# Kernel tuning notes

Measured on AMD Instinct MI355X. Metric: run time of the kernel, lower is better.

The kernel has to match this reference:

```python
import jax, jax.numpy as jnp
import numpy as np

B, T, N, CIN, C, L, NC, S = 8, 64, 200, 200, 128, 2, 2, 100
SPARSITY = 30


def bn(x, g, b, eps=1e-5):
    # BatchNorm1d forward with batch statistics (training-mode math, biased var)
    m = x.mean(0)
    v = x.var(0)
    return (x - m) / jnp.sqrt(v + eps) * g + b


def ln(x, g, b, eps=1e-5):
    m = x.mean(-1, keepdims=True)
    v = x.var(-1, keepdims=True)
    return (x - m) / jnp.sqrt(v + eps) * g + b


def setup_inputs() -> dict:
    key = jax.random.key(0)
    ks = iter(jax.random.split(key, 64))

    def nrm(shape, s=0.02):
        return jax.random.normal(next(ks), shape, jnp.float32) * s

    return dict(
        fMRI_v=jax.random.normal(next(ks), (B, T, N, CIN), jnp.float32),
        fMRI_a=jax.random.uniform(next(ks), (B, T, N, N), jnp.float32),
        sMRI_trad=jax.random.normal(next(ks), (B, S), jnp.float32),
        sMRI_deep=jnp.zeros((B, 1, 8, 8, 8), jnp.float32),
        csatt=1, CA_MOD=0,
        w_init=nrm((CIN, C)), b_init=jnp.zeros((C,), jnp.float32),
        gin_eps=jnp.zeros((L,), jnp.float32),
        gin_w1=nrm((L, C, C)), gin_b1=jnp.zeros((L, C), jnp.float32),
        gin_bn1_g=jnp.ones((L, C), jnp.float32), gin_bn1_b=jnp.zeros((L, C), jnp.float32),
        gin_w2=nrm((L, C, C)), gin_b2=jnp.zeros((L, C), jnp.float32),
        gin_bn2_g=jnp.ones((L, C), jnp.float32), gin_bn2_b=jnp.zeros((L, C), jnp.float32),
        sero_w=nrm((L, C, C)), sero_b=jnp.zeros((L, C), jnp.float32),
        sero_bn_g=jnp.ones((L, C), jnp.float32), sero_bn_b=jnp.zeros((L, C), jnp.float32),
        sero_aw=nrm((L, C, N)), sero_ab=jnp.zeros((L, N), jnp.float32),
        tr_wqkv=nrm((L, C, 3 * C)), tr_bqkv=jnp.zeros((L, 3 * C), jnp.float32),
        tr_wo=nrm((L, C, C)), tr_bo=jnp.zeros((L, C), jnp.float32),
        tr_ln1_g=jnp.ones((L, C), jnp.float32), tr_ln1_b=jnp.zeros((L, C), jnp.float32),
        tr_ln2_g=jnp.ones((L, C), jnp.float32), tr_ln2_b=jnp.zeros((L, C), jnp.float32),
        tr_w1=nrm((L, C, 2 * C)), tr_b1=jnp.zeros((L, 2 * C), jnp.float32),
        tr_w2=nrm((L, 2 * C, C)), tr_b2=jnp.zeros((L, C), jnp.float32),
        cls_w=nrm((L, C, NC)), cls_b=jnp.zeros((L, NC), jnp.float32),
        smri_w=nrm((S, C)), smri_b=jnp.zeros((C,), jnp.float32),
        smri_bn_g=jnp.ones((C,), jnp.float32), smri_bn_b=jnp.zeros((C,), jnp.float32),
    )


def reference(fMRI_v, fMRI_a, sMRI_trad, sMRI_deep, csatt, CA_MOD,
              w_init, b_init, gin_eps,
              gin_w1, gin_b1, gin_bn1_g, gin_bn1_b,
              gin_w2, gin_b2, gin_bn2_g, gin_bn2_b,
              sero_w, sero_b, sero_bn_g, sero_bn_b, sero_aw, sero_ab,
              tr_wqkv, tr_bqkv, tr_wo, tr_bo,
              tr_ln1_g, tr_ln1_b, tr_ln2_g, tr_ln2_b,
              tr_w1, tr_b1, tr_w2, tr_b2,
              cls_w, cls_b, smri_w, smri_b, smri_bn_g, smri_bn_b):
    b, t, n = fMRI_a.shape[:3]
    # initial linear over flattened (b t n) tokens
    h3 = (fMRI_v.reshape(-1, fMRI_v.shape[-1]) @ w_init + b_init).reshape(b, t, n, -1)
    # _collate_adjacency: per-(sample,timepoint) percentile threshold -> block-diag sparse
    # with all-ones values; equivalent to a batched masked matmul.
    thr = jnp.percentile(fMRI_a, 100 - SPARSITY, axis=(-2, -1), keepdims=True)
    mask = (fMRI_a > thr).astype(h3.dtype)  # [b,t,n,n]

    logit = jnp.zeros((b, cls_w.shape[-1]), h3.dtype)
    latents, node_attns, time_attns = [], [], []
    scale = 1.0 / jnp.sqrt(jnp.asarray(h3.shape[-1], h3.dtype))
    for l in range(L):
        # LayerGIN: note the original feeds h3 (initial features) to EVERY layer
        agg = jnp.einsum('btij,btjc->btic', mask, h3) + gin_eps[l] * h3
        x = agg.reshape(-1, agg.shape[-1])
        x = jax.nn.relu(bn(x @ gin_w1[l] + gin_b1[l], gin_bn1_g[l], gin_bn1_b[l]))
        x = jax.nn.relu(bn(x @ gin_w2[l] + gin_b2[l], gin_bn2_g[l], gin_bn2_b[l]))
        hb = x.reshape(b, t, n, -1).transpose(1, 0, 2, 3)  # (t,b,n,c)
        # ModuleSERO readout (node_axis=2)
        xr = hb.mean(2)  # (t,b,c)
        e = jax.nn.gelu(bn(xr.reshape(t * b, -1) @ sero_w[l] + sero_b[l],
                           sero_bn_g[l], sero_bn_b[l]), approximate=False)
        ga = jax.nn.sigmoid(e @ sero_aw[l] + sero_ab[l]).reshape(t, b, n)
        hr = (hb * ga[..., None]).mean(2)  # (t,b,c)
        node_attns.append(ga.transpose(1, 0, 2))  # (b,t,n)
        # ModuleTransformer (single head, post-LN, no residual before ln1)
        qkv = hr @ tr_wqkv[l] + tr_bqkv[l]
        q, k, v = jnp.split(qkv, 3, axis=-1)
        A = jax.nn.softmax(jnp.einsum('tbc,sbc->bts', q, k) * scale, axis=-1)  # (b,t,t)
        att = jnp.einsum('bts,sbc->tbc', A, v) @ tr_wo[l] + tr_bo[l]
        x1 = ln(att, tr_ln1_g[l], tr_ln1_b[l])
        m = jax.nn.relu(x1 @ tr_w1[l] + tr_b1[l]) @ tr_w2[l] + tr_b2[l]
        x2 = ln(x1 + m, tr_ln2_g[l], tr_ln2_b[l])
        time_attns.append(A)
        lat = x2.sum(0)  # cls_token='sum' over time
        logit = logit + lat @ cls_w[l] + cls_b[l]
        latents.append(lat)
    feat_fMRI = jnp.stack(latents, 1).mean(1)  # (b,c)
    feat_sMRI = bn(sMRI_trad @ smri_w + smri_b, smri_bn_g, smri_bn_b)
    node_attn = jnp.stack(node_attns, 1)  # (b,L,t,n)
    time_attn = jnp.stack(time_attns, 1)  # (b,L,t,t)
    return (logit, feat_fMRI, feat_sMRI, node_attn, time_attn)
```

## Files before the change

### kernel.cpp

```cpp
#include <hip/hip_runtime.h>
#include <math.h>

#define B_   8
#define T_   64
#define N_   200
#define CIN_ 200
#define C_   128
#define L_   2
#define NC_  2
#define S_   100
#define BT_  512
#define RB_  102400

#define ACT_NONE 0
#define ACT_RELU 1
#define ACT_GELU 2

typedef __attribute__((ext_vector_type(8))) short short8v;
typedef __attribute__((ext_vector_type(4))) float f32x4v;

union U4S8 { uint4 u; short8v s; };

__device__ __forceinline__ unsigned short f2bf(float f) {
    unsigned u = __float_as_uint(f);
// ... 75 lines not shown
                    float f = vv[j];
                    if (p < 6144) { candV[p] = f; candP[p] = (unsigned short)(i4 * 4 + j); }
                    int bin = (int)((f - 0.65f) * 10240.0f);
                    bin = bin < 0 ? 0 : (bin > 1023 ? 1023 : bin);
                    atomicAdd(&hist[bin], 1);
                    p++;
                }
            }
        }
    }
    red[tid] = c_lo;
    __syncthreads();
    for (int off = 512; off; off >>= 1) {
        if (tid < off) red[tid] += red[tid + off];
        __syncthreads();
    }
    int c_lo_tot = red[0];
    if (tid < 256) part[tid] = hist[4*tid] + hist[4*tid+1] + hist[4*tid+2] + hist[4*tid+3];
    __syncthreads();
    if (tid < 32) {
        int s = 0;
        for (int i = 0; i < 8; i++) s += part[8*tid + i];
        grp[tid] = s;
    }
    __syncthreads();
    if (tid == 0) {
        int r = 27999 - c_lo_tot;
        int cum = 0, g = 0;
        while (cum + grp[g] <= r) cum += grp[g++];
        int t = g * 8;
        while (cum + part[t] <= r) cum += part[t++];
        int b = t * 4;
        while (cum + hist[b] <= r) cum += hist[b++];
        meta[2] = b; meta[3] = cum;
        int r1 = r + 1;
        cum = 0; g = 0;
        while (cum + grp[g] <= r1) cum += grp[g++];
        t = g * 8;
        while (cum + part[t] <= r1) cum += part[t++];
        b = t * 4;
        while (cum + hist[b] <= r1) cum += hist[b++];
        meta[4] = b; meta[5] = r;
    }
    __syncthreads();
    int blo = meta[2], base = meta[3], bhi = meta[4], r = meta[5];
    int m = meta[0]; if (m > 6144) m = 6144;
    for (int i = tid; i < m; i += 1024) {
        float v = candV[i];
        int bin = (int)((v - 0.65f) * 10240.0f);
        bin = bin < 0 ? 0 : (bin > 1023 ? 1023 : bin);
        if (bin >= blo && bin <= bhi) {
            int p = atomicAdd(&meta[1], 1);
            if (p < 256) cand2[p] = v;
        }
    }
    __syncthreads();
    if (tid == 0) {
        int m2 = meta[1]; if (m2 > 256) m2 = 256;
        for (int i = 1; i < m2; i++) {
            float key = cand2[i]; int j = i - 1;
            while (j >= 0 && cand2[j] > key) { cand2[j+1] = cand2[j]; j--; }
            cand2[j+1] = key;
        }
        float s1 = cand2[r - base], s2 = cand2[r + 1 - base];
        float tv = s1 * 0.701171875f + s2 * 0.298828125f;
        thr[bt] = tv;
        s_thr = tv;
    }
    __syncthreads();
    float tv = s_thr;
    for (int i = tid; i < m; i += 1024) {
        if (candV[i] > tv) {
            int vi = candP[i];
            int row = vi / 200, col = vi - row * 200;
            atomicOr(&smask[row * 7 + (col >> 5)], 1u << (col & 31));
        }
    }
    __syncthreads();
    for (int i = tid; i < 1400; i += 1024)
        msk[(long)bt * 1400 + i] = smask[i];
}

__global__ void wtcvt_kernel(const float* __restrict__ w, int K, int Kpad,
                             unsigned short* __restrict__ wt) {
    int c = blockIdx.x;
    for (int k = threadIdx.x; k < Kpad; k += 64) {
        float v = (k < K) ? w[(long)k * 128 + c] : 0.f;
        wt[(long)c * Kpad + k] = f2bf(v);
    }
}

template<bool A_BF16, bool BN_IN, bool BIAS_OUT, bool STATS_OUT>
__global__ __launch_bounds__(256) void gemm_direct_kernel(
        const void* __restrict__ xv, int K, int Kstride, int Ksteps,
        const unsigned short* __restrict__ wt, int Kpad,
        const float* __restrict__ bias, const float* __restrict__ statsIn,
        const float* __restrict__ bng, const float* __restrict__ bnb,
        unsigned short* __restrict__ y, float* __restrict__ statsOut) {
    constexpr int ASZ  = A_BF16 ? 8192 : 16384;
    constexpr int BOFF = 2 * ASZ;
    constexpr int NEED = 2 * ASZ + 2 * 8192;
    constexpr int POOL = NEED > 32768 ? NEED : 32768;
    __shared__ unsigned char pool[POOL];
    __shared__ float bnS[128], bnB[128];
    int tid = threadIdx.x;
    if (BN_IN) {
        if (tid < 128) {
            float mm = statsIn[tid] * (1.f / (float)RB_);
            float var = fmaxf(statsIn[128 + tid] * (1.f / (float)RB_) - mm * mm, 0.f);
            float sc = bng[tid] / sqrtf(var + 1e-5f);
            bnS[tid] = sc; bnB[tid] = bnb[tid] - mm * sc;
        }
    }
    int wave = tid >> 6, lane = tid & 63, quad = lane >> 4, m16 = lane & 15;
    long row0g = (long)blockIdx.x * 128;

    auto STAGE = [&](int buf, int ks) {
        #pragma unroll
        for (int j = 0; j < 2; j++) {
            int r = j * 64 + (tid >> 2);
            int c = (tid & 3) ^ ((r >> 1) & 3);
            const char* src = (const char*)wt + (long)r * (Kpad * 2) + ks * 64 + c * 16;
            char* dst = (char*)pool + BOFF + buf * 8192 + j * 4096 + wave * 1024;
            GLL(src, dst);
        }
        if (A_BF16) {
            const char* xb = (const char*)xv;
            #pragma unroll
            for (int j = 0; j < 2; j++) {
                int r = j * 64 + (tid >> 2);
                int c = (tid & 3) ^ ((r >> 1) & 3);
                const char* src = xb + ((row0g + r) * Kstride + ks * 32) * 2 + c * 16;
                char* dst = (char*)pool + buf * ASZ + j * 4096 + wave * 1024;
                GLL(src, dst);
            }
        } else {
            const char* xb = (const char*)xv;
            #pragma unroll
            for (int j = 0; j < 4; j++) {
                int r = j * 32 + (tid >> 3);
                int c = (tid & 7) ^ (r & 7);
                const char* src = xb + ((row0g + r) * Kstride + ks * 32) * 4 + c * 16;
                char* dst = (char*)pool + buf * ASZ + j * 4096 + wave * 1024;
                GLL(src, dst);
            }
        }
    };

    f32x4v acc[2][8];
    #pragma unroll
    for (int i = 0; i < 2; i++)
        #pragma unroll
        for (int j = 0; j < 8; j++) acc[i][j] = (f32x4v){0.f, 0.f, 0.f, 0.f};

    STAGE(0, 0);
    __syncthreads();

    for (int ks = 0; ks < Ksteps; ks++) {
        if (ks + 1 < Ksteps) {
            STAGE((ks + 1) & 1, ks + 1);
            if (A_BF16) asm volatile("s_waitcnt vmcnt(4)" ::: "memory");
            else        asm volatile("s_waitcnt vmcnt(6)" ::: "memory");
        } else {
            asm volatile("s_waitcnt vmcnt(0)" ::: "memory");
        }
        __builtin_amdgcn_s_barrier();
        asm volatile("" ::: "memory");

        const char* Ab = (const char*)pool + (ks & 1) * ASZ;
        const char* Bb = (const char*)pool + BOFF + (ks & 1) * 8192;
        int kf = ks * 32 + quad * 8;
        U4S8 bU[8];
        #pragma unroll
        for (int nt = 0; nt < 8; nt++) {
            int r = nt * 16 + m16;
            int ch = quad ^ ((r >> 1) & 3);
            bU[nt].u = *(const uint4*)(Bb + r * 64 + ch * 16);
        }
        U4S8 aU[2];
        if (A_BF16) {
            #pragma unroll
            for (int mt = 0; mt < 2; mt++) {
                int r = wave * 32 + mt * 16 + m16;
                int ch = quad ^ ((r >> 1) & 3);
                aU[mt].u = *(const uint4*)(Ab + r * 64 + ch * 16);
            }
            if (BN_IN) {
                float4 s0 = *(const float4*)&bnS[kf], s1 = *(const float4*)&bnS[kf + 4];
                float4 b0 = *(const float4*)&bnB[kf], b1 = *(const float4*)&bnB[kf + 4];
                #pragma unroll
                for (int mt = 0; mt < 2; mt++) {
                    uint4 u = aU[mt].u;
                    float f0 = fmaxf(bflo(u.x) * s0.x + b0.x, 0.f);
                    float f1 = fmaxf(bfhi(u.x) * s0.y + b0.y, 0.f);
                    float f2 = fmaxf(bflo(u.y) * s0.z + b0.z, 0.f);
                    float f3 = fmaxf(bfhi(u.y) * s0.w + b0.w, 0.f);
                    float f4 = fmaxf(bflo(u.z) * s1.x + b1.x, 0.f);
                    float f5 = fmaxf(bfhi(u.z) * s1.y + b1.y, 0.f);
                    float f6 = fmaxf(bflo(u.w) * s1.z + b1.z, 0.f);
                    float f7 = fmaxf(bfhi(u.w) * s1.w + b1.w, 0.f);
                    u.x = packbf(f0, f1); u.y = packbf(f2, f3);
                    u.z = packbf(f4, f5); u.w = packbf(f6, f7);
                    aU[mt].u = u;
                }
            }
        } else {
            #pragma unroll
            for (int mt = 0; mt < 2; mt++) {
                int r = wave * 32 + mt * 16 + m16;
                int swz = r & 7;
                const char* base = Ab + r * 128;
                float4 v0 = *(const float4*)(base + ((2 * quad) ^ swz) * 16);
                float4 v1 = *(const float4*)(base + ((2 * quad + 1) ^ swz) * 16);
                uint4 o;
                o.x = packbf(v0.x, v0.y); o.y = packbf(v0.z, v0.w);
                o.z = packbf(v1.x, v1.y); o.w = packbf(v1.z, v1.w);
                aU[mt].u = o;
            }
        }
        #pragma unroll
        for (int nt = 0; nt < 8; nt++) {
            acc[0][nt] = __builtin_amdgcn_mfma_f32_16x16x32_bf16(aU[0].s, bU[nt].s, acc[0][nt], 0, 0, 0);
            acc[1][nt] = __builtin_amdgcn_mfma_f32_16x16x32_bf16(aU[1].s, bU[nt].s, acc[1][nt], 0, 0, 0);
        }
        asm volatile("s_waitcnt lgkmcnt(0)" ::: "memory");
        __builtin_amdgcn_s_barrier();
        asm volatile("" ::: "memory");
    }
    if (!A_BF16 && (K & 31) != 0) {
        int kf = Ksteps * 32 + quad * 8;
        U4S8 bU[8];
        #pragma unroll
        for (int nt = 0; nt < 8; nt++)
            bU[nt].u = *(const uint4*)&wt[(long)(nt * 16 + m16) * Kpad + kf];
        U4S8 aU[2];
        const float* x = (const float*)xv;
        #pragma unroll
        for (int mt = 0; mt < 2; mt++) {
            uint4 o = {0u, 0u, 0u, 0u};
            if (kf + 8 <= K) {
                const float* p = &x[(row0g + wave * 32 + mt * 16 + m16) * Kstride + kf];
                float4 v0 = *(const float4*)p;
                float4 v1 = *(const float4*)(p + 4);
                o.x = packbf(v0.x, v0.y); o.y = packbf(v0.z, v0.w);
                o.z = packbf(v1.x, v1.y); o.w = packbf(v1.z, v1.w);
            }
            aU[mt].u = o;
        }
        #pragma unroll
        for (int nt = 0; nt < 8; nt++) {
            acc[0][nt] = __builtin_amdgcn_mfma_f32_16x16x32_bf16(aU[0].s, bU[nt].s, acc[0][nt], 0, 0, 0);
            acc[1][nt] = __builtin_amdgcn_mfma_f32_16x16x32_bf16(aU[1].s, bU[nt].s, acc[1][nt], 0, 0, 0);
        }
    }

    unsigned short* trans = (unsigned short*)pool;
    float sAcc[8], qAcc[8];
    #pragma unroll
    for (int nt = 0; nt < 8; nt++) {
        int col = nt * 16 + m16;
        float bv = BIAS_OUT ? bias[col] : 0.f;
        float s = 0.f, q = 0.f;
        #pragma unroll
        for (int mt = 0; mt < 2; mt++) {
            int lrb = wave * 32 + mt * 16 + quad * 4;
            #pragma unroll
            for (int i = 0; i < 4; i++) {
                int lr = lrb + i;
                float v = acc[mt][nt][i] + bv;
                trans[lr * 128 + (col ^ ((lr & 6) << 2))] = f2bf(v);
                if (STATS_OUT) { s += v; q += v * v; }
            }
        }
        sAcc[nt] = s; qAcc[nt] = q;
    }
    __syncthreads();
    #pragma unroll
    for (int rnd = 0; rnd < 8; rnd++) {
        int row = rnd * 16 + (tid >> 4), ch = tid & 15;
        uint4 v = *(const uint4*)&trans[row * 128 + ((ch * 8) ^ ((row & 6) << 2))];
        *(uint4*)&y[(row0g + row) * 128 + ch * 8] = v;
    }
    if (STATS_OUT) {
        __syncthreads();
        float* redS = (float*)pool;
        float* redQ = redS + 2048;
        #pragma unroll
        for (int nt = 0; nt < 8; nt++) {
            int col = nt * 16 + m16;
            redS[col * 16 + wave * 4 + quad] = sAcc[nt];
            redQ[col * 16 + wave * 4 + quad] = qAcc[nt];
        }
        __syncthreads();
        if (tid < 128) {
            float s = 0.f, q = 0.f;
            #pragma unroll
            for (int j = 0; j < 16; j++) { s += redS[tid * 16 + j]; q += redQ[tid * 16 + j]; }
            atomicAdd(&statsOut[tid], s);
            atomicAdd(&statsOut[128 + tid], q);
        }
    }
}

__global__ __launch_bounds__(256) void gemmT_kernel(
        const unsigned short* __restrict__ xb, const unsigned short* __restrict__ wt,
        unsigned short* __restrict__ zt) {
    __shared__ unsigned char pool[32768];
    int tid = threadIdx.x;
    int wave = tid >> 6, lane = tid & 63, quad = lane >> 4, m16 = lane & 15;
    long row0g = (long)blockIdx.x * 128;

    auto STAGE = [&](int buf, int ks) {
        #pragma unroll
        for (int j = 0; j < 2; j++) {
            int r = j * 64 + (tid >> 2);
            int c = (tid & 3) ^ ((r >> 1) & 3);
            const char* srcB = (const char*)wt + (long)r * 256 + ks * 64 + c * 16;
            char* dstB = (char*)pool + 16384 + buf * 8192 + j * 4096 + wave * 1024;
            GLL(srcB, dstB);
            const char* srcA = (const char*)xb + ((row0g + r) * 128 + ks * 32) * 2 + c * 16;
            char* dstA = (char*)pool + buf * 8192 + j * 4096 + wave * 1024;
            GLL(srcA, dstA);
        }
    };

    f32x4v acc[2][8];
    #pragma unroll
    for (int i = 0; i < 2; i++)
        #pragma unroll
        for (int j = 0; j < 8; j++) acc[i][j] = (f32x4v){0.f, 0.f, 0.f, 0.f};

    STAGE(0, 0);
    __syncthreads();

    for (int ks = 0; ks < 4; ks++) {
        if (ks < 3) {
            STAGE((ks + 1) & 1, ks + 1);
            asm volatile("s_waitcnt vmcnt(4)" ::: "memory");
        } else {
            asm volatile("s_waitcnt vmcnt(0)" ::: "memory");
        }
        __builtin_amdgcn_s_barrier();
        asm volatile("" ::: "memory");

        const char* Ab = (const char*)pool + (ks & 1) * 8192;
        const char* Bb = (const char*)pool + 16384 + (ks & 1) * 8192;
        U4S8 bU[8];
        #pragma unroll
        for (int nt = 0; nt < 8; nt++) {
            int r = nt * 16 + m16;
            int ch = quad ^ ((r >> 1) & 3);
            bU[nt].u = *(const uint4*)(Bb + r * 64 + ch * 16);
        }
        U4S8 aU[2];
        #pragma unroll
        for (int mt = 0; mt < 2; mt++) {
            int r = wave * 32 + mt * 16 + m16;
            int ch = quad ^ ((r >> 1) & 3);
            aU[mt].u = *(const uint4*)(Ab + r * 64 + ch * 16);
        }
        #pragma unroll
        for (int nt = 0; nt < 8; nt++) {
            acc[0][nt] = __builtin_amdgcn_mfma_f32_16x16x32_bf16(aU[0].s, bU[nt].s, acc[0][nt], 0, 0, 0);
            acc[1][nt] = __builtin_amdgcn_mfma_f32_16x16x32_bf16(aU[1].s, bU[nt].s, acc[1][nt], 0, 0, 0);
        }
        asm volatile("s_waitcnt lgkmcnt(0)" ::: "memory");
        __builtin_amdgcn_s_barrier();
        asm volatile("" ::: "memory");
    }
    unsigned short* tile = (unsigned short*)pool;
    #pragma unroll
    for (int nt = 0; nt < 8; nt++) {
        int col = nt * 16 + m16;
        #pragma unroll
        for (int mt = 0; mt < 2; mt++) {
            int lrb = wave * 32 + mt * 16 + quad * 4;
            #pragma unroll
            for (int i = 0; i < 4; i++) {
                int lr = lrb + i;
                tile[lr * 128 + (col ^ ((lr & 14) << 2))] = f2bf(acc[mt][nt][i]);
            }
        }
    }
    __syncthreads();
    int r0 = blockIdx.x * 128;
    int bt0 = r0 / 200, n0 = r0 - bt0 * 200;
    int len0 = 200 - n0; if (len0 > 128) len0 = 128;
    int c = tid & 127, h = tid >> 7;
    #pragma unroll
    for (int u = 0; u < 8; u++) {
        int rl = h * 64 + u * 8;
        unsigned short e[8];
        #pragma unroll
        for (int j = 0; j < 8; j++)
            e[j] = tile[(rl + j) * 128 + (c ^ (((rl + j) & 14) << 2))];
        uint4 o;
        o.x = (unsigned)e[0] | ((unsigned)e[1] << 16);
        o.y = (unsigned)e[2] | ((unsigned)e[3] << 16);
        o.z = (unsigned)e[4] | ((unsigned)e[5] << 16);
        o.w = (unsigned)e[6] | ((unsigned)e[7] << 16);
        int bt, n;
        if (rl < len0) { bt = bt0; n = n0 + rl; } else { bt = bt0 + 1; n = rl - len0; }
        *(uint4*)&zt[((long)bt * 128 + c) * 224 + n] = o;
    }
    if (n0 >= 72) {
        uint4 z = {0u, 0u, 0u, 0u};
        for (int idx = tid; idx < 384; idx += 256) {
            int c2 = idx & 127, u2 = idx >> 7;
            *(uint4*)&zt[((long)bt0 * 128 + c2) * 224 + 200 + u2 * 8] = z;
        }
    }
}

__global__ __launch_bounds__(256) void maskagg_kernel(
        const unsigned* __restrict__ msk, const unsigned short* __restrict__ zt,
        const float* __restrict__ geps, int l, const float* __restrict__ b1,
        unsigned short* __restrict__ y, float* __restrict__ statsOut) {
    __shared__ union {
        unsigned short stage[4][4096];
        unsigned short trans[16384];
        struct { float S[2048]; float Q[2048]; } red;
    } u;
    __shared__ unsigned sbits[128 * 7];
    int tid = threadIdx.x;
    int bt = blockIdx.x & 511, half = blockIdx.x >> 9;
    int row0 = half * 128;
    int wave = tid >> 6, lane = tid & 63, quad = lane >> 4, m16 = lane & 15;
    const char* ztb = (const char*)(zt + (long)bt * 128 * 224);

    int sr = tid >> 2, sq = tid & 3;
    auto STAGE = [&](int buf, int kc) {
        #pragma unroll
        for (int j = 0; j < 2; j++) {
            int r = j * 64 + sr;
            int q = sq ^ ((r >> 1) & 3);
            const char* src = ztb + r * 448 + kc * 64 + q * 16;
            char* dst = (char*)&u.stage[buf][0] + j * 4096 + wave * 1024;
            GLL(src, dst);
        }
    };

    STAGE(0, 0); STAGE(1, 1); STAGE(2, 2);
    for (int idx = tid; idx < 896; idx += 256) {
        int gr = row0 + idx / 7;
        sbits[idx] = (gr < N_) ? msk[(long)bt * 1400 + gr * 7 + (idx % 7)] : 0u;
    }
    float eps = geps[l];
    unsigned ONEu = 0x3F80u;
    unsigned E0 = (unsigned)f2bf(eps), E1 = (unsigned)f2bf(1.f + eps);

    f32x4v acc[2][8];
    #pragma unroll
    for (int i = 0; i < 2; i++)
        #pragma unroll
        for (int j = 0; j < 8; j++) acc[i][j] = (f32x4v){0.f, 0.f, 0.f, 0.f};

    __syncthreads();

    for (int kc = 0; kc < 7; kc++) {
        if (kc < 4) STAGE((kc + 3) & 3, kc + 3);
        if (kc == 3)      asm volatile("s_waitcnt vmcnt(6)" ::: "memory");
        else if (kc == 4) asm volatile("s_waitcnt vmcnt(4)" ::: "memory");
        else if (kc == 5) asm volatile("s_waitcnt vmcnt(2)" ::: "memory");
        else if (kc == 6) asm volatile("s_waitcnt vmcnt(0)" ::: "memory");
        __builtin_amdgcn_s_barrier();
        asm volatile("" ::: "memory");

        const char* sb = (const char*)&u.stage[kc & 3][0];
        int kf = kc * 32 + quad * 8;
        U4S8 bU[8];
        #pragma unroll
        for (int nt = 0; nt < 8; nt++) {
            int r = nt * 16 + m16;
            int q = quad ^ ((r >> 1) & 3);
            bU[nt].u = *(const uint4*)(sb + r * 64 + q * 16);
        }
        U4S8 aU[2];
        #pragma unroll
        for (int mt = 0; mt < 2; mt++) {
            int lr = wave * 32 + mt * 16 + m16;
            unsigned bits = (sbits[lr * 7 + kc] >> (quad * 8)) & 0xFFu;
            int gr = row0 + lr;
            unsigned o[4];
            #pragma unroll
            for (int p = 0; p < 4; p++) {
                int j0 = 2 * p, j1 = 2 * p + 1;
                unsigned lo = ((bits >> j0) & 1u) ? ONEu : 0u;
                unsigned hi = ((bits >> j1) & 1u) ? ONEu : 0u;
                if (gr == kf + j0) lo = ((bits >> j0) & 1u) ? E1 : E0;
                if (gr == kf + j1) hi = ((bits >> j1) & 1u) ? E1 : E0;
                o[p] = lo | (hi << 16);
            }
            aU[mt].u = make_uint4(o[0], o[1], o[2], o[3]);
        }
        #pragma unroll
        for (int nt = 0; nt < 8; nt++) {
            acc[0][nt] = __builtin_amdgcn_mfma_f32_16x16x32_bf16(aU[0].s, bU[nt].s, acc[0][nt], 0, 0, 0);
            acc[1][nt] = __builtin_amdgcn_mfma_f32_16x16x32_bf16(aU[1].s, bU[nt].s, acc[1][nt], 0, 0, 0);
        }
        asm volatile("s_waitcnt lgkmcnt(0)" ::: "memory");
        __builtin_amdgcn_s_barrier();
        asm volatile("" ::: "memory");
    }

    float sAcc[8], qAcc[8];
    #pragma unroll
    for (int nt = 0; nt < 8; nt++) {
        int col = nt * 16 + m16;
        float bv = b1[col];
        float s = 0.f, q = 0.f;
        #pragma unroll
        for (int mt = 0; mt < 2; mt++) {
            int lrb = wave * 32 + mt * 16 + quad * 4;
            #pragma unroll
            for (int i = 0; i < 4; i++) {
                int lr = lrb + i;
                float v = acc[mt][nt][i] + bv;
                u.trans[lr * 128 + (col ^ ((lr & 6) << 2))] = f2bf(v);
                if (row0 + lr < N_) { s += v; q += v * v; }
            }
        }
        sAcc[nt] = s; qAcc[nt] = q;
    }
    __syncthreads();
    #pragma unroll
    for (int rnd = 0; rnd < 8; rnd++) {
        int row = rnd * 16 + (tid >> 4), ch = tid & 15;
        int gr = row0 + row;
        uint4 v = *(const uint4*)&u.trans[row * 128 + ((ch * 8) ^ ((row & 6) << 2))];
        if (gr < N_)
            *(uint4*)&y[((long)bt * N_ + gr) * 128 + ch * 8] = v;
    }
    __syncthreads();
    #pragma unroll
    for (int nt = 0; nt < 8; nt++) {
        int col = nt * 16 + m16;
        u.red.S[col * 16 + wave * 4 + quad] = sAcc[nt];
        u.red.Q[col * 16 + wave * 4 + quad] = qAcc[nt];
    }
    __syncthreads();
    if (tid < 128) {
        float s = 0.f, q = 0.f;
        #pragma unroll
        for (int j = 0; j < 16; j++) { s += u.red.S[tid * 16 + j]; q += u.red.Q[tid * 16 + j]; }
        atomicAdd(&statsOut[tid], s);
        atomicAdd(&statsOut[128 + tid], q);
    }
}

__global__ __launch_bounds__(128) void xr2_kernel(const unsigned short* __restrict__ raw,
                                                  const float* __restrict__ stats,
                                                  const float* __restrict__ g,
                                                  const float* __restrict__ b,
                                                  float* __restrict__ xr) {
    int t = blockIdx.x / B_, bb = blockIdx.x % B_;
    const unsigned short* base = raw + ((long)bb * T_ + t) * N_ * C_;
    int c = threadIdx.x;
    float m = stats[c] * (1.f / (float)RB_);
    float var = fmaxf(stats[128 + c] * (1.f / (float)RB_) - m * m, 0.f);
    float sc = g[c] / sqrtf(var + 1e-5f);
    float sh = b[c] - m * sc;
    float s = 0.f;
    for (int n = 0; n < N_; n++) s += fmaxf(fmaf(bf2f(base[n * C_ + c]), sc, sh), 0.f);
    xr[(long)blockIdx.x * C_ + c] = s * (1.f / 200.f);
}

__global__ __launch_bounds__(128) void hr2_kernel(const unsigned short* __restrict__ raw,
                                                  const float* __restrict__ stats,
                                                  const float* __restrict__ g,
                                                  const float* __restrict__ b,
                                                  const float* __restrict__ ga,
                                                  float* __restrict__ hr) {
    __shared__ float sga[N_];
    int t = blockIdx.x / B_, bb = blockIdx.x % B_;
    const unsigned short* base = raw + ((long)bb * T_ + t) * N_ * C_;
    for (int i = threadIdx.x; i < N_; i += blockDim.x) sga[i] = ga[(long)blockIdx.x * N_ + i];
    __syncthreads();
    int c = threadIdx.x;
    float m = stats[c] * (1.f / (float)RB_);
    float var = fmaxf(stats[128 + c] * (1.f / (float)RB_) - m * m, 0.f);
    float sc = g[c] / sqrtf(var + 1e-5f);
    float sh = b[c] - m * sc;
    float s = 0.f;
    for (int n = 0; n < N_; n++)
        s = fmaf(fmaxf(fmaf(bf2f(base[n * C_ + c]), sc, sh), 0.f), sga[n], s);
    hr[(long)blockIdx.x * C_ + c] = s * (1.f / 200.f);
}

template<int K, int ROWS, bool STATS>
__global__ void mm_kernel(const float* __restrict__ x, const float* __restrict__ w,
                          const float* __restrict__ bias, float* __restrict__ y,
                          int Cout, int act, float* __restrict__ stats) {
    __shared__ float sx[ROWS * K];
    long r0 = (long)blockIdx.x * ROWS;
    for (int idx = threadIdx.x; idx < ROWS * K; idx += blockDim.x)
        sx[idx] = x[r0 * K + idx];
    __syncthreads();
    int c = threadIdx.x;
    float acc[ROWS];
    #pragma unroll
    for (int i = 0; i < ROWS; i++) acc[i] = 0.f;
    for (int k = 0; k < K; k++) {
        float wv = w[k * Cout + c];
        #pragma unroll
        for (int i = 0; i < ROWS; i++) acc[i] = fmaf(sx[i * K + k], wv, acc[i]);
    }
    float bv = bias ? bias[c] : 0.f;
    float s = 0.f, ss = 0.f;
    for (int i = 0; i < ROWS; i++) {
        float vv = acc[i] + bv;
        if (act == ACT_RELU) vv = fmaxf(vv, 0.f);
        y[(r0 + i) * Cout + c] = vv;
        if (STATS) { s += vv; ss += vv * vv; }
    }
    if (STATS) {
        atomicAdd(&stats[c], s);
        atomicAdd(&stats[C_ + c], ss);
    }
}

__global__ __launch_bounds__(256) void ga_kernel(const float* __restrict__ eRaw,
                          const float* __restrict__ stats,
                          const float* __restrict__ sg, const float* __restrict__ sb,
                          const float* __restrict__ aw, const float* __restrict__ ab,
                          float* __restrict__ ga, float* __restrict__ node_out, int l) {
    __shared__ float sx[4 * C_];
    __shared__ float bnS[C_], bnB[C_];
    int tid = threadIdx.x;
    if (tid < C_) {
        float m = stats[tid] * (1.f / (float)BT_);
        float var = fmaxf(stats[C_ + tid] * (1.f / (float)BT_) - m * m, 0.f);
        float inv = 1.f / sqrtf(var + 1e-5f);
        float sc = inv * sg[tid];
        bnS[tid] = sc;
        bnB[tid] = sb[tid] - m * sc;
    }
    __syncthreads();
    long r0 = (long)blockIdx.x * 4;
    for (int idx = tid; idx < 4 * C_; idx += 256) {
        int col = idx & (C_ - 1);
        float v = eRaw[r0 * C_ + idx] * bnS[col] + bnB[col];
        sx[idx] = 0.5f * v * (1.f + erff(v * 0.70710678118654752f));
    }
    __syncthreads();
    int c = tid;
    if (c < N_) {
        float acc[4] = {0.f, 0.f, 0.f, 0.f};
        for (int k = 0; k < C_; k++) {
            float wv = aw[k * N_ + c];
            #pragma unroll
            for (int i = 0; i < 4; i++) acc[i] = fmaf(sx[i * C_ + k], wv, acc[i]);
        }
        float bv = ab[c];
        for (int i = 0; i < 4; i++) {
            int tb = (int)r0 + i;
            int t = tb / B_, b = tb % B_;
            float v = 1.f / (1.f + expf(-(acc[i] + bv)));
            ga[(long)tb * N_ + c] = v;
            node_out[(((long)b * L_ + l) * T_ + t) * N_ + c] = v;
        }
    }
}

__global__ __launch_bounds__(128) void attnav_kernel(const float* __restrict__ qkv,
                            float* __restrict__ time_out, float* __restrict__ attv, int l) {
    __shared__ float q[C_];
    __shared__ float sa[T_];
    int tid = threadIdx.x;
    int t = blockIdx.x / B_, b = blockIdx.x % B_;
    q[tid] = qkv[((long)t * B_ + b) * 384 + tid];
    __syncthreads();
    if (tid < 64) {
        const float* krow = qkv + ((long)tid * B_ + b) * 384 + C_;
        float s = 0.f;
        for (int c = 0; c < C_; c++) s = fmaf(q[c], krow[c], s);
        s *= 0.08838834764831843f;
        float mx = s;
        #pragma unroll
        for (int off = 32; off; off >>= 1) mx = fmaxf(mx, __shfl_xor(mx, off));
        float e = expf(s - mx), sum = e;
        #pragma unroll
        for (int off = 32; off; off >>= 1) sum += __shfl_xor(sum, off);
        float p = e / sum;
        sa[tid] = p;
        time_out[(((long)b * L_ + l) * T_ + t) * T_ + tid] = p;
    }
    __syncthreads();
    float s2 = 0.f;
    for (int sp = 0; sp < T_; sp++)
        s2 = fmaf(sa[sp], qkv[((long)sp * B_ + b) * 384 + 256 + tid], s2);
    attv[((long)t * B_ + b) * C_ + tid] = s2;
}

__global__ __launch_bounds__(128) void mmln_kernel(const float* __restrict__ x,
                          const float* __restrict__ w, const float* __restrict__ bias,
                          const float* __restrict__ g, const float* __restrict__ bb,
                          float* __restrict__ out) {
    __shared__ float sx[2 * C_];
    __shared__ float red[C_];
    int tid = threadIdx.x;
    long r0 = (long)blockIdx.x * 2;
    sx[tid]       = x[r0 * C_ + tid];
    sx[C_ + tid]  = x[r0 * C_ + C_ + tid];
    __syncthreads();
    float a0 = 0.f, a1 = 0.f;
    for (int k = 0; k < C_; k++) {
        float wv = w[k * C_ + tid];
        a0 = fmaf(sx[k], wv, a0);
        a1 = fmaf(sx[C_ + k], wv, a1);
    }
    float bv = bias[tid];
    float v[2] = {a0 + bv, a1 + bv};
    #pragma unroll 1
    for (int r = 0; r < 2; r++) {
        red[tid] = v[r]; __syncthreads();
        for (int off = 64; off; off >>= 1) { if (tid < off) red[tid] += red[tid + off]; __syncthreads(); }
        float m = red[0] * (1.f / C_); __syncthreads();
        float d = v[r] - m;
        red[tid] = d * d; __syncthreads();
        for (int off = 64; off; off >>= 1) { if (tid < off) red[tid] += red[tid + off]; __syncthreads(); }
        float var = red[0] * (1.f / C_); __syncthreads();
        out[(r0 + r) * C_ + tid] = d * (1.f / sqrtf(var + 1e-5f)) * g[tid] + bb[tid];
    }
}

__global__ __launch_bounds__(256) void ffn_kernel(const float* __restrict__ x1,
                          const float* __restrict__ w1, const float* __restrict__ b1,
                          const float* __restrict__ w2, const float* __restrict__ b2,
                          const float* __restrict__ g, const float* __restrict__ bb,
                          float* __restrict__ out) {
    __shared__ float sx[2 * C_];
    __shared__ float mid[2 * 256];
    __shared__ float red[C_];
    int tid = threadIdx.x;
    long r0 = (long)blockIdx.x * 2;
    sx[tid] = x1[r0 * C_ + tid];
    __syncthreads();
    float a0 = 0.f, a1 = 0.f;
    for (int k = 0; k < C_; k++) {
        float wv = w1[k * 256 + tid];
        a0 = fmaf(sx[k], wv, a0);
        a1 = fmaf(sx[C_ + k], wv, a1);
    }
    float bv = b1[tid];
    mid[tid]       = fmaxf(a0 + bv, 0.f);
    mid[256 + tid] = fmaxf(a1 + bv, 0.f);
    __syncthreads();
    float v[2] = {0.f, 0.f};
    if (tid < C_) {
        float c0 = 0.f, c1 = 0.f;
        for (int k = 0; k < 256; k++) {
            float wv = w2[k * C_ + tid];
            c0 = fmaf(mid[k], wv, c0);
            c1 = fmaf(mid[256 + k], wv, c1);
        }
        float bv2 = b2[tid];
        v[0] = c0 + bv2 + sx[tid];
        v[1] = c1 + bv2 + sx[C_ + tid];
    }
    #pragma unroll 1
    for (int r = 0; r < 2; r++) {
        if (tid < C_) red[tid] = v[r];
        __syncthreads();
        for (int off = 64; off; off >>= 1) { if (tid < off) red[tid] += red[tid + off]; __syncthreads(); }
        float m = red[0] * (1.f / C_); __syncthreads();
        float d = v[r] - m;
        if (tid < C_) red[tid] = d * d;
        __syncthreads();
        for (int off = 64; off; off >>= 1) { if (tid < off) red[tid] += red[tid + off]; __syncthreads(); }
        float var = red[0] * (1.f / C_); __syncthreads();
        if (tid < C_)
            out[(r0 + r) * C_ + tid] = d * (1.f / sqrtf(var + 1e-5f)) * g[tid] + bb[tid];
    }
}

__global__ void latsum_kernel(const float* __restrict__ x2, float* __restrict__ lat) {
    int b = blockIdx.x, c = threadIdx.x;
    float s = 0.f;
    for (int t = 0; t < T_; t++) s += x2[((long)t * B_ + b) * C_ + c];
    lat[(long)b * C_ + c] = s;
}

__global__ void final_kernel(const float* __restrict__ lat, const float* __restrict__ cls_w,
                             const float* __restrict__ cls_b, float* __restrict__ out) {
    int idx = blockIdx.x * blockDim.x + threadIdx.x;
    if (idx < B_ * NC_) {
        int b = idx / NC_, nc = idx % NC_;
        float s = 0.f;
        for (int l = 0; l < L_; l++) {
            float acc = 0.f;
            for (int c = 0; c < C_; c++)
                acc = fmaf(lat[l * B_ * C_ + b * C_ + c], cls_w[l * C_ * NC_ + c * NC_ + nc], acc);
            s += acc + cls_b[l * NC_ + nc];
        }
        out[idx] = s;
    } else if (idx < B_ * NC_ + B_ * C_) {
        int j = idx - B_ * NC_;
        out[idx] = 0.5f * (lat[j] + lat[B_ * C_ + j]);
    }
}

__global__ void smri_kernel(const float* __restrict__ trad, const float* __restrict__ w,
                            const float* __restrict__ bias, const float* __restrict__ g,
                            const float* __restrict__ bb, float* __restrict__ out) {
    int c = threadIdx.x;
    float y[B_];
    for (int b = 0; b < B_; b++) {
        float s = bias[c];
        for (int k = 0; k < S_; k++) s = fmaf(trad[b * S_ + k], w[k * C_ + c], s);
        y[b] = s;
    }
    float m = 0.f;
    for (int b = 0; b < B_; b++) m += y[b];
    m *= (1.f / B_);
    float var = 0.f;
    for (int b = 0; b < B_; b++) { float d = y[b] - m; var += d * d; }
    var *= (1.f / B_);
    float inv = 1.f / sqrtf(var + 1e-5f);
    for (int b = 0; b < B_; b++) out[b * C_ + c] = (y[b] - m) * inv * g[c] + bb[c];
}

extern "C" void kernel_launch(void* const* d_in, const int* in_sizes, int n_in,
                              void* d_out, int out_size, void* d_ws, size_t ws_size,
                              hipStream_t stream) {
    const float* fv       = (const float*)d_in[0];
    const float* fa       = (const float*)d_in[1];
    const float* trad     = (const float*)d_in[2];
    const float* w_init   = (const float*)d_in[6];
    const float* b_init   = (const float*)d_in[7];
    const float* gin_eps  = (const float*)d_in[8];
    const float* gin_w1   = (const float*)d_in[9];
    const float* gin_b1   = (const float*)d_in[10];
    const float* gbn1g    = (const float*)d_in[11];
    const float* gbn1b    = (const float*)d_in[12];
    const float* gin_w2   = (const float*)d_in[13];
    const float* gin_b2   = (const float*)d_in[14];
    const float* gbn2g    = (const float*)d_in[15];
    const float* gbn2b    = (const float*)d_in[16];
    const float* sero_w   = (const float*)d_in[17];
    const float* sero_b   = (const float*)d_in[18];
    const float* sbng     = (const float*)d_in[19];
    const float* sbnb     = (const float*)d_in[20];
    const float* sero_aw  = (const float*)d_in[21];
    const float* sero_ab  = (const float*)d_in[22];
    const float* wqkv     = (const float*)d_in[23];
    const float* bqkv     = (const float*)d_in[24];
    const float* wo       = (const float*)d_in[25];
    const float* bo       = (const float*)d_in[26];
    const float* ln1g     = (const float*)d_in[27];
    const float* ln1b     = (const float*)d_in[28];
    const float* ln2g     = (const float*)d_in[29];
    const float* ln2b     = (const float*)d_in[30];
    const float* tw1      = (const float*)d_in[31];
    const float* tb1      = (const float*)d_in[32];
    const float* tw2      = (const float*)d_in[33];
    const float* tb2      = (const float*)d_in[34];
    const float* cls_w    = (const float*)d_in[35];
    const float* cls_b    = (const float*)d_in[36];
    const float* smri_w   = (const float*)d_in[37];
    const float* smri_b   = (const float*)d_in[38];
    const float* smri_g   = (const float*)d_in[39];
    const float* smri_bb  = (const float*)d_in[40];

    float* out = (float*)d_out;

    const long SZ_BIG = (long)RB_ * C_;
    unsigned short* H3b = (unsigned short*)d_ws;
    unsigned short* Y1b = H3b + SZ_BIG;
    unsigned short* Y2b = Y1b + SZ_BIG;
    unsigned short* ZTb = Y2b + SZ_BIG;
    float* fbase = (float*)(ZTb + (long)BT_ * 128 * 224);
    float* THR  = fbase;
    float* STAT = THR + 512;
    float* XR   = STAT + 256;
    float* E    = XR  + BT_ * C_;
    float* GA   = E   + BT_ * C_;
    float* HR   = GA  + BT_ * N_;
    float* QKV  = HR  + BT_ * C_;
    float* ATTV = QKV + BT_ * 3 * C_;
    float* ATT  = ATTV + BT_ * C_;
    float* X1   = ATT + BT_ * C_;
    float* MMB  = X1  + BT_ * C_;
    float* X2   = MMB + BT_ * 2 * C_;
    float* LAT  = X2  + BT_ * C_;
    float* STATB = MMB;
    unsigned short* WT0 = (unsigned short*)(LAT + L_ * B_ * C_);
    unsigned short* WT1 = WT0 + 128 * 224;
    unsigned short* WT2 = WT1 + 2 * 128 * 128;
    unsigned* MSK = (unsigned*)(WT2 + 2 * 128 * 128);

    float* OUT_LOGIT = out;
    float* OUT_FEATS = out + 1040;
    float* OUT_NODE  = out + 2064;
    float* OUT_TIME  = out + 206864;

    wtcvt_kernel<<<128, 64, 0, stream>>>(w_init, 200, 224, WT0);
    wtcvt_kernel<<<128, 64, 0, stream>>>(gin_w1,           128, 128, WT1);
    wtcvt_kernel<<<128, 64, 0, stream>>>(gin_w1 + C_ * C_, 128, 128, WT1 + 128 * 128);
    wtcvt_kernel<<<128, 64, 0, stream>>>(gin_w2,           128, 128, WT2);
    wtcvt_kernel<<<128, 64, 0, stream>>>(gin_w2 + C_ * C_, 128, 128, WT2 + 128 * 128);

    gemm_direct_kernel<false, false, true, false><<<RB_ / 128, 256, 0, stream>>>(
        fv, 200, 200, 6, WT0, 224, b_init, nullptr, nullptr, nullptr, H3b, nullptr);
    thr_kernel<<<BT_, 1024, 0, stream>>>(fa, THR, MSK);

    for (int l = 0; l < L_; l++) {
        gemmT_kernel<<<RB_ / 128, 256, 0, stream>>>(H3b, WT1 + l * 128 * 128, ZTb);
        hipMemsetAsync(STAT, 0, 256 * sizeof(float), stream);
        maskagg_kernel<<<BT_ * 2, 256, 0, stream>>>(MSK, ZTb, gin_eps, l, gin_b1 + l * C_, Y2b, STAT);
        hipMemsetAsync(STATB, 0, 256 * sizeof(float), stream);
        gemm_direct_kernel<true, true, true, true><<<RB_ / 128, 256, 0, stream>>>(
            Y2b, 128, 128, 4, WT2 + l * 128 * 128, 128, gin_b2 + l * C_, STAT,
            gbn1g + l * C_, gbn1b + l * C_, Y1b, STATB);
        xr2_kernel<<<BT_, 128, 0, stream>>>(Y1b, STATB, gbn2g + l * C_, gbn2b + l * C_, XR);

        hipMemsetAsync(STAT, 0, 256 * sizeof(float), stream);
        mm_kernel<128, 2, true><<<BT_ / 2, 128, 0, stream>>>(
            XR, sero_w + l * C_ * C_, sero_b + l * C_, E, C_, ACT_NONE, STAT);
        ga_kernel<<<BT_ / 4, 256, 0, stream>>>(E, STAT, sbng + l * C_, sbnb + l * C_,
            sero_aw + l * C_ * N_, sero_ab + l * N_, GA, OUT_NODE, l);
        hr2_kernel<<<BT_, 128, 0, stream>>>(Y1b, STATB, gbn2g + l * C_, gbn2b + l * C_, GA, HR);

        mm_kernel<128, 2, false><<<BT_ / 2, 384, 0, stream>>>(
            HR, wqkv + l * C_ * 3 * C_, bqkv + l * 3 * C_, QKV, 3 * C_, ACT_NONE, nullptr);
        attnav_kernel<<<BT_, 128, 0, stream>>>(QKV, OUT_TIME, ATTV, l);
        mmln_kernel<<<BT_ / 2, 128, 0, stream>>>(ATTV, wo + l * C_ * C_, bo + l * C_,
            ln1g + l * C_, ln1b + l * C_, X1);
        ffn_kernel<<<BT_ / 2, 256, 0, stream>>>(X1, tw1 + l * C_ * 2 * C_, tb1 + l * 2 * C_,
            tw2 + l * 2 * C_ * C_, tb2 + l * C_, ln2g + l * C_, ln2b + l * C_, X2);
        latsum_kernel<<<B_, 128, 0, stream>>>(X2, LAT + l * B_ * C_);
    }

    final_kernel<<<5, 256, 0, stream>>>(LAT, cls_w, cls_b, OUT_LOGIT);
    smri_kernel<<<1, 128, 0, stream>>>(trad, smri_w, smri_b, smri_g, smri_bb, OUT_FEATS);
}
```

Before: 778.2 us.

## Aggregate node features before the GIN weight matmul and fuse it into the mask kernel

The GIN step now aggregates first, computing (A + eps·I)·H3 with the binary mask, and only then multiplies by W1, instead of computing H3·W1 first. The initial feature GEMM converts fp32 input to bf16 in-kernel and writes both the row-major and the transposed H3, which removes the per-layer transpose-GEMM launch. The W1 GEMM, the eps·H3 self term and the bias are fused into the mask-aggregation kernel, reading W1 and H3 from global memory. Separately, the two node-mean reduction kernels now use 256 threads, with each half summing 100 nodes. The tradeoff is an extra bf16 rounding of the aggregate before W1, plus uncached global loads inside the fused kernel.

```diff
diff --git a/kernel.cpp b/kernel.cpp
--- a/kernel.cpp
+++ b/kernel.cpp
@@ -401,10 +401,11 @@
     }
 }
 
-__global__ __launch_bounds__(256) void gemmT_kernel(
-        const unsigned short* __restrict__ xb, const unsigned short* __restrict__ wt,
-        unsigned short* __restrict__ zt) {
-    __shared__ unsigned char pool[32768];
+__global__ __launch_bounds__(256) void h3gemmT_kernel(
+        const float* __restrict__ xv, const unsigned short* __restrict__ wt,
+        const float* __restrict__ bias,
+        unsigned short* __restrict__ yrow, unsigned short* __restrict__ zt) {
+    __shared__ unsigned char pool[49152];
     int tid = threadIdx.x;
     int wave = tid >> 6, lane = tid & 63, quad = lane >> 4, m16 = lane & 15;
     long row0g = (long)blockIdx.x * 128;
@@ -414,12 +415,18 @@
         for (int j = 0; j < 2; j++) {
             int r = j * 64 + (tid >> 2);
             int c = (tid & 3) ^ ((r >> 1) & 3);
-            const char* srcB = (const char*)wt + (long)r * 256 + ks * 64 + c * 16;
-            char* dstB = (char*)pool + 16384 + buf * 8192 + j * 4096 + wave * 1024;
-            GLL(srcB, dstB);
-            const char* srcA = (const char*)xb + ((row0g + r) * 128 + ks * 32) * 2 + c * 16;
-            char* dstA = (char*)pool + buf * 8192 + j * 4096 + wave * 1024;
-            GLL(srcA, dstA);
+            const char* src = (const char*)wt + (long)r * 448 + ks * 64 + c * 16;
+            char* dst = (char*)pool + 32768 + buf * 8192 + j * 4096 + wave * 1024;
+            GLL(src, dst);
+        }
+        const char* xb = (const char*)xv;
+        #pragma unroll
+        for (int j = 0; j < 4; j++) {
+            int r = j * 32 + (tid >> 3);
+            int c = (tid & 7) ^ (r & 7);
+            const char* src = xb + ((row0g + r) * 200 + ks * 32) * 4 + c * 16;
+            char* dst = (char*)pool + buf * 16384 + j * 4096 + wave * 1024;
+            GLL(src, dst);
         }
     };
 
@@ -432,18 +439,18 @@
     STAGE(0, 0);
     __syncthreads();
 
-    for (int ks = 0; ks < 4; ks++) {
-        if (ks < 3) {
+    for (int ks = 0; ks < 6; ks++) {
+        if (ks + 1 < 6) {
             STAGE((ks + 1) & 1, ks + 1);
-            asm volatile("s_waitcnt vmcnt(4)" ::: "memory");
+            asm volatile("s_waitcnt vmcnt(6)" ::: "memory");
         } else {
             asm volatile("s_waitcnt vmcnt(0)" ::: "memory");
         }
         __builtin_amdgcn_s_barrier();
         asm volatile("" ::: "memory");
 
-        const char* Ab = (const char*)pool + (ks & 1) * 8192;
-        const char* Bb = (const char*)pool + 16384 + (ks & 1) * 8192;
+        const char* Ab = (const char*)pool + (ks & 1) * 16384;
+        const char* Bb = (const char*)pool + 32768 + (ks & 1) * 8192;
         U4S8 bU[8];
         #pragma unroll
         for (int nt = 0; nt < 8; nt++) {
@@ -455,8 +462,14 @@
         #pragma unroll
         for (int mt = 0; mt < 2; mt++) {
             int r = wave * 32 + mt * 16 + m16;
-            int ch = quad ^ ((r >> 1) & 3);
-            aU[mt].u = *(const uint4*)(Ab + r * 64 + ch * 16);
+            int swz = r & 7;
+            const char* base = Ab + r * 128;
+            float4 v0 = *(const float4*)(base + ((2 * quad) ^ swz) * 16);
+            float4 v1 = *(const float4*)(base + ((2 * quad + 1) ^ swz) * 16);
+            uint4 o;
+            o.x = packbf(v0.x, v0.y); o.y = packbf(v0.z, v0.w);
+            o.z = packbf(v1.x, v1.y); o.w = packbf(v1.z, v1.w);
+            aU[mt].u = o;
         }
         #pragma unroll
         for (int nt = 0; nt < 8; nt++) {
@@ -467,21 +480,54 @@
         __builtin_amdgcn_s_barrier();
         asm volatile("" ::: "memory");
     }
+    {
+        int kf = 192 + quad * 8;
+        U4S8 bU[8];
+        #pragma unroll
+        for (int nt = 0; nt < 8; nt++)
+            bU[nt].u = *(const uint4*)&wt[(long)(nt * 16 + m16) * 224 + kf];
+        U4S8 aU[2];
+        #pragma unroll
+        for (int mt = 0; mt < 2; mt++) {
+            uint4 o = {0u, 0u, 0u, 0u};
+            if (kf + 8 <= 200) {
+                const float* p = &xv[(row0g + wave * 32 + mt * 16 + m16) * 200 + kf];
+                float4 v0 = *(const float4*)p;
+                float4 v1 = *(const float4*)(p + 4);
+                o.x = packbf(v0.x, v0.y); o.y = packbf(v0.z, v0.w);
+                o.z = packbf(v1.x, v1.y); o.w = packbf(v1.z, v1.w);
+            }
+            aU[mt].u = o;
+        }
+        #pragma unroll
+        for (int nt = 0; nt < 8; nt++) {
+            acc[0][nt] = __builtin_amdgcn_mfma_f32_16x16x32_bf16(aU[0].s, bU[nt].s, acc[0][nt], 0, 0, 0);
+            acc[1][nt] = __builtin_amdgcn_mfma_f32_16x16x32_bf16(aU[1].s, bU[nt].s, acc[1][nt], 0, 0, 0);
+        }
+    }
+
     unsigned short* tile = (unsigned short*)pool;
     #pragma unroll
     for (int nt = 0; nt < 8; nt++) {
         int col = nt * 16 + m16;
+        float bv = bias[col];
         #pragma unroll
         for (int mt = 0; mt < 2; mt++) {
             int lrb = wave * 32 + mt * 16 + quad * 4;
             #pragma unroll
             for (int i = 0; i < 4; i++) {
                 int lr = lrb + i;
-                tile[lr * 128 + (col ^ ((lr & 14) << 2))] = f2bf(acc[mt][nt][i]);
-            }
-        }
-    }
-    __syncthreads();
+                tile[lr * 128 + (col ^ ((lr & 14) << 2))] = f2bf(acc[mt][nt][i] + bv);
+            }
+        }
+    }
+    __syncthreads();
+    #pragma unroll
+    for (int rnd = 0; rnd < 8; rnd++) {
+        int row = rnd * 16 + (tid >> 4), ch = tid & 15;
+        uint4 v = *(const uint4*)&tile[row * 128 + ((ch * 8) ^ ((row & 14) << 2))];
+        *(uint4*)&yrow[(row0g + row) * 128 + ch * 8] = v;
+    }
     int r0 = blockIdx.x * 128;
     int bt0 = r0 / 200, n0 = r0 - bt0 * 200;
     int len0 = 200 - n0; if (len0 > 128) len0 = 128;
@@ -511,8 +557,9 @@
     }
 }
 
-__global__ __launch_bounds__(256) void maskagg_kernel(
+__global__ __launch_bounds__(256) void maskfused_kernel(
         const unsigned* __restrict__ msk, const unsigned short* __restrict__ zt,
+        const unsigned short* __restrict__ h3, const unsigned short* __restrict__ w1t,
         const float* __restrict__ geps, int l, const float* __restrict__ b1,
         unsigned short* __restrict__ y, float* __restrict__ statsOut) {
     __shared__ union {
@@ -544,9 +591,7 @@
         int gr = row0 + idx / 7;
         sbits[idx] = (gr < N_) ? msk[(long)bt * 1400 + gr * 7 + (idx % 7)] : 0u;
     }
-    float eps = geps[l];
     unsigned ONEu = 0x3F80u;
-    unsigned E0 = (unsigned)f2bf(eps), E1 = (unsigned)f2bf(1.f + eps);
 
     f32x4v acc[2][8];
     #pragma unroll
@@ -566,7 +611,6 @@
         asm volatile("" ::: "memory");
 
         const char* sb = (const char*)&u.stage[kc & 3][0];
-        int kf = kc * 32 + quad * 8;
         U4S8 bU[8];
         #pragma unroll
         for (int nt = 0; nt < 8; nt++) {
@@ -579,15 +623,11 @@
         for (int mt = 0; mt < 2; mt++) {
             int lr = wave * 32 + mt * 16 + m16;
             unsigned bits = (sbits[lr * 7 + kc] >> (quad * 8)) & 0xFFu;
-            int gr = row0 + lr;
             unsigned o[4];
             #pragma unroll
             for (int p = 0; p < 4; p++) {
-                int j0 = 2 * p, j1 = 2 * p + 1;
-                unsigned lo = ((bits >> j0) & 1u) ? ONEu : 0u;
-                unsigned hi = ((bits >> j1) & 1u) ? ONEu : 0u;
-                if (gr == kf + j0) lo = ((bits >> j0) & 1u) ? E1 : E0;
-                if (gr == kf + j1) hi = ((bits >> j1) & 1u) ? E1 : E0;
+                unsigned lo = ((bits >> (2 * p)) & 1u) ? ONEu : 0u;
+                unsigned hi = ((bits >> (2 * p + 1)) & 1u) ? ONEu : 0u;
                 o[p] = lo | (hi << 16);
             }
             aU[mt].u = make_uint4(o[0], o[1], o[2], o[3]);
@@ -601,6 +641,63 @@
         __builtin_amdgcn_s_barrier();
         asm volatile("" ::: "memory");
     }
+
+    #pragma unroll
+    for (int nt = 0; nt < 8; nt++) {
+        int col = nt * 16 + m16;
+        #pragma unroll
+        for (int mt = 0; mt < 2; mt++) {
+            int lrb = wave * 32 + mt * 16 + quad * 4;
+            #pragma unroll
+            for (int i = 0; i < 4; i++) {
+                int lr = lrb + i;
+                u.trans[lr * 128 + (col ^ ((lr & 6) << 2))] = f2bf(acc[mt][nt][i]);
+            }
+        }
+    }
+    __syncthreads();
+
+    float eps = geps[l];
+    f32x4v acc2[2][8];
+    #pragma unroll
+    for (int i = 0; i < 2; i++)
+        #pragma unroll
+        for (int j = 0; j < 8; j++) acc2[i][j] = (f32x4v){0.f, 0.f, 0.f, 0.f};
+
+    for (int ks = 0; ks < 4; ks++) {
+        int kf = ks * 32 + quad * 8;
+        U4S8 bU[8];
+        #pragma unroll
+        for (int nt = 0; nt < 8; nt++)
+            bU[nt].u = *(const uint4*)&w1t[(long)(nt * 16 + m16) * 128 + kf];
+        U4S8 aU[2];
+        #pragma unroll
+        for (int mt = 0; mt < 2; mt++) {
+            int r = wave * 32 + mt * 16 + m16;
+            uint4 mu = *(const uint4*)&u.trans[r * 128 + (kf ^ ((r & 6) << 2))];
+            int gr = row0 + r;
+            uint4 hu = {0u, 0u, 0u, 0u};
+            if (gr < N_) hu = *(const uint4*)&h3[((long)bt * N_ + gr) * 128 + kf];
+            float f0 = bflo(mu.x) + eps * bflo(hu.x);
+            float f1 = bfhi(mu.x) + eps * bfhi(hu.x);
+            float f2 = bflo(mu.y) + eps * bflo(hu.y);
+            float f3 = bfhi(mu.y) + eps * bfhi(hu.y);
+            float f4 = bflo(mu.z) + eps * bflo(hu.z);
+            float f5 = bfhi(mu.z) + eps * bfhi(hu.z);
+            float f6 = bflo(mu.w) + eps * bflo(hu.w);
+            float f7 = bfhi(mu.w) + eps * bfhi(hu.w);
+            uint4 o;
+            o.x = packbf(f0, f1); o.y = packbf(f2, f3);
+            o.z = packbf(f4, f5); o.w = packbf(f6, f7);
+            aU[mt].u = o;
+        }
+        #pragma unroll
+        for (int nt = 0; nt < 8; nt++) {
+            acc2[0][nt] = __builtin_amdgcn_mfma_f32_16x16x32_bf16(aU[0].s, bU[nt].s, acc2[0][nt], 0, 0, 0);
+            acc2[1][nt] = __builtin_amdgcn_mfma_f32_16x16x32_bf16(aU[1].s, bU[nt].s, acc2[1][nt], 0, 0, 0);
+        }
+    }
+    __syncthreads();
 
     float sAcc[8], qAcc[8];
     #pragma unroll
@@ -614,7 +711,7 @@
             #pragma unroll
             for (int i = 0; i < 4; i++) {
                 int lr = lrb + i;
-                float v = acc[mt][nt][i] + bv;
+                float v = acc2[mt][nt][i] + bv;
                 u.trans[lr * 128 + (col ^ ((lr & 6) << 2))] = f2bf(v);
                 if (row0 + lr < N_) { s += v; q += v * v; }
             }
@@ -647,43 +744,52 @@
     }
 }
 
-__global__ __launch_bounds__(128) void xr2_kernel(const unsigned short* __restrict__ raw,
+__global__ __launch_bounds__(256) void xr2_kernel(const unsigned short* __restrict__ raw,
                                                   const float* __restrict__ stats,
                                                   const float* __restrict__ g,
                                                   const float* __restrict__ b,
                                                   float* __restrict__ xr) {
+    __shared__ float red[256];
+    int tid = threadIdx.x, c = tid & 127, hf = tid >> 7;
     int t = blockIdx.x / B_, bb = blockIdx.x % B_;
     const unsigned short* base = raw + ((long)bb * T_ + t) * N_ * C_;
-    int c = threadIdx.x;
     float m = stats[c] * (1.f / (float)RB_);
     float var = fmaxf(stats[128 + c] * (1.f / (float)RB_) - m * m, 0.f);
     float sc = g[c] / sqrtf(var + 1e-5f);
     float sh = b[c] - m * sc;
     float s = 0.f;
-    for (int n = 0; n < N_; n++) s += fmaxf(fmaf(bf2f(base[n * C_ + c]), sc, sh), 0.f);
-    xr[(long)blockIdx.x * C_ + c] = s * (1.f / 200.f);
-}
-
-__global__ __launch_bounds__(128) void hr2_kernel(const unsigned short* __restrict__ raw,
+    for (int n = hf * 100; n < hf * 100 + 100; n++)
+        s += fmaxf(fmaf(bf2f(base[n * C_ + c]), sc, sh), 0.f);
+    red[tid] = s;
+    __syncthreads();
+    if (hf == 0)
+        xr[(long)blockIdx.x * C_ + c] = (red[c] + red[c + 128]) * (1.f / 200.f);
+}
+
+__global__ __launch_bounds__(256) void hr2_kernel(const unsigned short* __restrict__ raw,
                                                   const float* __restrict__ stats,
                                                   const float* __restrict__ g,
                                                   const float* __restrict__ b,
                                                   const float* __restrict__ ga,
                                                   float* __restrict__ hr) {
     __shared__ float sga[N_];
+    __shared__ float red[256];
+    int tid = threadIdx.x, c = tid & 127, hf = tid >> 7;
     int t = blockIdx.x / B_, bb = blockIdx.x % B_;
     const unsigned short* base = raw + ((long)bb * T_ + t) * N_ * C_;
-    for (int i = threadIdx.x; i < N_; i += blockDim.x) sga[i] = ga[(long)blockIdx.x * N_ + i];
-    __syncthreads();
-    int c = threadIdx.x;
+    for (int i = tid; i < N_; i += 256) sga[i] = ga[(long)blockIdx.x * N_ + i];
+    __syncthreads();
     float m = stats[c] * (1.f / (float)RB_);
     float var = fmaxf(stats[128 + c] * (1.f / (float)RB_) - m * m, 0.f);
     float sc = g[c] / sqrtf(var + 1e-5f);
     float sh = b[c] - m * sc;
     float s = 0.f;
-    for (int n = 0; n < N_; n++)
+    for (int n = hf * 100; n < hf * 100 + 100; n++)
         s = fmaf(fmaxf(fmaf(bf2f(base[n * C_ + c]), sc, sh), 0.f), sga[n], s);
-    hr[(long)blockIdx.x * C_ + c] = s * (1.f / 200.f);
+    red[tid] = s;
+    __syncthreads();
+    if (hf == 0)
+        hr[(long)blockIdx.x * C_ + c] = (red[c] + red[c + 128]) * (1.f / 200.f);
 }
 
 template<int K, int ROWS, bool STATS>
@@ -999,26 +1105,25 @@
     wtcvt_kernel<<<128, 64, 0, stream>>>(gin_w2,           128, 128, WT2);
     wtcvt_kernel<<<128, 64, 0, stream>>>(gin_w2 + C_ * C_, 128, 128, WT2 + 128 * 128);
 
-    gemm_direct_kernel<false, false, true, false><<<RB_ / 128, 256, 0, stream>>>(
-        fv, 200, 200, 6, WT0, 224, b_init, nullptr, nullptr, nullptr, H3b, nullptr);
+    h3gemmT_kernel<<<RB_ / 128, 256, 0, stream>>>(fv, WT0, b_init, H3b, ZTb);
     thr_kernel<<<BT_, 1024, 0, stream>>>(fa, THR, MSK);
 
     for (int l = 0; l < L_; l++) {
-        gemmT_kernel<<<RB_ / 128, 256, 0, stream>>>(H3b, WT1 + l * 128 * 128, ZTb);
         hipMemsetAsync(STAT, 0, 256 * sizeof(float), stream);
-        maskagg_kernel<<<BT_ * 2, 256, 0, stream>>>(MSK, ZTb, gin_eps, l, gin_b1 + l * C_, Y2b, STAT);
+        maskfused_kernel<<<BT_ * 2, 256, 0, stream>>>(MSK, ZTb, H3b, WT1 + l * 128 * 128,
+            gin_eps, l, gin_b1 + l * C_, Y2b, STAT);
         hipMemsetAsync(STATB, 0, 256 * sizeof(float), stream);
         gemm_direct_kernel<true, true, true, true><<<RB_ / 128, 256, 0, stream>>>(
             Y2b, 128, 128, 4, WT2 + l * 128 * 128, 128, gin_b2 + l * C_, STAT,
             gbn1g + l * C_, gbn1b + l * C_, Y1b, STATB);
-        xr2_kernel<<<BT_, 128, 0, stream>>>(Y1b, STATB, gbn2g + l * C_, gbn2b + l * C_, XR);
+        xr2_kernel<<<BT_, 256, 0, stream>>>(Y1b, STATB, gbn2g + l * C_, gbn2b + l * C_, XR);
 
         hipMemsetAsync(STAT, 0, 256 * sizeof(float), stream);
         mm_kernel<128, 2, true><<<BT_ / 2, 128, 0, stream>>>(
             XR, sero_w + l * C_ * C_, sero_b + l * C_, E, C_, ACT_NONE, STAT);
         ga_kernel<<<BT_ / 4, 256, 0, stream>>>(E, STAT, sbng + l * C_, sbnb + l * C_,
             sero_aw + l * C_ * N_, sero_ab + l * N_, GA, OUT_NODE, l);
-        hr2_kernel<<<BT_, 128, 0, stream>>>(Y1b, STATB, gbn2g + l * C_, gbn2b + l * C_, GA, HR);
+        hr2_kernel<<<BT_, 256, 0, stream>>>(Y1b, STATB, gbn2g + l * C_, gbn2b + l * C_, GA, HR);
 
         mm_kernel<128, 2, false><<<BT_ / 2, 384, 0, stream>>>(
             HR, wqkv + l * C_ * 3 * C_, bqkv + l * 3 * C_, QKV, 3 * C_, ACT_NONE, nullptr);
```

Result: no change. 773.6 us (-0.6%).
